# Kernel optimization log

Measured on AMD Instinct MI355X. Metric: run time of the kernel, lower is better.

Reference implementation:

```python
import jax, jax.numpy as jnp
import numpy as np

EPS = 1e-8  # CosineSimilarity eps
T = 0.5     # temperature


def _neg_indices(B):
    # static boolean mask removing diag and +/-B off-diagonals, as flat indices
    N = 2 * B
    m = np.eye(N) + np.eye(N, k=B) + np.eye(N, k=-B)
    mask = (1 - m).astype(bool)
    return np.nonzero(mask.ravel())[0]  # shape [N*(N-2)]


def setup_inputs() -> dict:
    key = jax.random.key(0)
    k1, k2 = jax.random.split(key)
    B, D = 4096, 128
    proj_i = jax.random.normal(k1, (B, D), dtype=jnp.float32)
    proj_j = jax.random.normal(k2, (B, D), dtype=jnp.float32)
    return {"proj_i": proj_i, "proj_j": proj_j}


def reference(proj_i, proj_j):
    B = proj_i.shape[0]
    N = 2 * B
    p = jnp.concatenate([proj_i, proj_j], axis=0)  # [N, D]
    # cosine sim of normalized vectors == dot product of unit vectors
    z = p / jnp.maximum(jnp.linalg.norm(p, axis=1, keepdims=True), EPS)
    sim = z @ z.T  # [N, N]
    pos = jnp.concatenate([jnp.diagonal(sim, offset=B), jnp.diagonal(sim, offset=-B)])  # [N]
    neg_idx = jnp.asarray(_neg_indices(B))
    neg = sim.ravel()[neg_idx].reshape(N, N - 2)
    logits = jnp.concatenate([pos[:, None], neg], axis=1) / T  # [N, N-1]
    # cross-entropy with label 0, sum reduction, divided by N
    logp = jax.nn.log_softmax(logits, axis=-1)
    loss = -jnp.sum(logp[:, 0]) / N
    return loss
```

## Files before the change

### kernel.cpp

```cpp
#include <hip/hip_runtime.h>
#include <hip/hip_bf16.h>

typedef __attribute__((ext_vector_type(8))) short short8;
typedef __attribute__((ext_vector_type(4))) float f32x4;

#define N_TOT 8192
#define HALF_B 4096
#define D 128
#define BM 128
#define BN 128
#define NQ 8
#define SLICE (N_TOT / NQ)
#define NSTEP (SLICE / BN)
#define SCALE 1.6986437f
#define CDIAG 7.3890561f

#if __has_builtin(__builtin_amdgcn_exp2f)
  #define EXP2(x) __builtin_amdgcn_exp2f(x)
#else
  #define EXP2(x) exp2f(x)
#endif

static __device__ inline unsigned short f2bf(float f) {
    unsigned int u = __builtin_bit_cast(unsigned int, f);
    u = (u + 0x7fffu + ((u >> 16) & 1u)) >> 16;
    return (unsigned short)u;
}

static __device__ __forceinline__ void gload16(const void* g, void* l) {
    __builtin_amdgcn_global_load_lds(
        (const __attribute__((address_space(1))) unsigned int*)g,
        (__attribute__((address_space(3))) unsigned int*)l, 16, 0, 0);
}

static __device__ __forceinline__ void stage_tile(const unsigned short* __restrict__ z,
                                                  int src_row, char* ldsbase, int tid) {
    int wv = tid >> 6, ln = tid & 63;
    const char* zb = (const char*)z;
    #pragma unroll
    for (int i = 0; i < 8; ++i) {
        int L  = wv * 8192 + i * 1024;
        int Ll = L + ln * 16;
        int r  = Ll >> 8;
        int c2 = (Ll & 255) ^ ((r & 15) << 4);
        gload16(zb + (size_t)(src_row + r) * 256 + c2, ldsbase + L);
    }
}

static __device__ __forceinline__ short8 ldsfrag(const char* ldsbase, int row, int kbyte) {
    int off = row * 256 + (kbyte ^ ((row & 15) << 4));
    return *reinterpret_cast<const short8*>(ldsbase + off);
}

__global__ __launch_bounds__(256) void nrm_k(const float* __restrict__ pi,
                                             const float* __restrict__ pj,
                                             unsigned short* __restrict__ z,
                                             float* __restrict__ ppos) {
    int tid = (int)threadIdx.x;
    int wid = tid >> 6, lane = tid & 63;
    int r = (int)blockIdx.x * 4 + wid;
    float2 va = *reinterpret_cast<const float2*>(pi + (size_t)r * D + lane * 2);
    float2 vb = *reinterpret_cast<const float2*>(pj + (size_t)r * D + lane * 2);
    float ssa = va.x * va.x + va.y * va.y;
    float ssb = vb.x * vb.x + vb.y * vb.y;
    float sab = va.x * vb.x + va.y * vb.y;
    #pragma unroll
    for (int off = 32; off >= 1; off >>= 1) {
        ssa += __shfl_xor(ssa, off);
        ssb += __shfl_xor(ssb, off);
        sab += __shfl_xor(sab, off);
    }
    float na = fmaxf(sqrtf(ssa), 1e-8f);
    float nb = fmaxf(sqrtf(ssb), 1e-8f);
    float inva = SCALE / na, invb = SCALE / nb;
    unsigned int pa = ((unsigned int)f2bf(va.y * inva) << 16) | (unsigned int)f2bf(va.x * inva);
    unsigned int pb = ((unsigned int)f2bf(vb.y * invb) << 16) | (unsigned int)f2bf(vb.x * invb);
    *reinterpret_cast<unsigned int*>(z + (size_t)r * D + lane * 2) = pa;
    *reinterpret_cast<unsigned int*>(z + (size_t)(r + HALF_B) * D + lane * 2) = pb;
    if (lane == 0) ppos[r] = 2.0f * sab / (na * nb);
}

__global__ __launch_bounds__(256, 2) void sim_k(const unsigned short* __restrict__ z,
                                                float* __restrict__ s_part) {
    __shared__ char lds[64 * 1024];
    char* Asm = lds;
    char* Bsm = lds + 32768;

    int tid  = (int)threadIdx.x;
    int lane = tid & 63;
    int wid  = tid >> 6;
    int lr   = lane & 15;
    int kg   = lane >> 4;
    int R0   = (int)blockIdx.x * BM;
    int C0   = (int)blockIdx.y * SLICE;

    stage_tile(z, R0, Asm, tid);
    stage_tile(z, C0, Bsm, tid);
    __syncthreads();

    short8 a[2][4];
    #pragma unroll
    for (int m = 0; m < 2; ++m)
        #pragma unroll
        for (int kt = 0; kt < 4; ++kt)
            a[m][kt] = ldsfrag(Asm, wid * 32 + m * 16 + lr, kg * 16 + kt * 64);

    float s[2][4];
    #pragma unroll
    for (int m = 0; m < 2; ++m)
        #pragma unroll
        for (int r = 0; r < 4; ++r) s[m][r] = 0.0f;

    for (int bs = 0; bs < NSTEP; ++bs) {
        if (bs) {
            __syncthreads();
            stage_tile(z, C0 + bs * BN, Bsm, tid);
            __syncthreads();
        }
        #pragma unroll
        for (int nt = 0; nt < 8; ++nt) {
            short8 b[4];
            #pragma unroll
            for (int kt = 0; kt < 4; ++kt)
                b[kt] = ldsfrag(Bsm, nt * 16 + lr, kg * 16 + kt * 64);
            #pragma unroll
            for (int m = 0; m < 2; ++m) {
                f32x4 acc = {0.0f, 0.0f, 0.0f, 0.0f};
                #pragma unroll
                for (int kt = 0; kt < 4; ++kt)
                    acc = __builtin_amdgcn_mfma_f32_16x16x32_bf16(a[m][kt], b[kt], acc, 0, 0, 0);
                #pragma unroll
                for (int r = 0; r < 4; ++r)
                    s[m][r] += EXP2(acc[r]);
            }
        }
    }

    #pragma unroll
    for (int off = 1; off <= 8; off <<= 1)
        #pragma unroll
        for (int m = 0; m < 2; ++m)
            #pragma unroll
            for (int r = 0; r < 4; ++r)
                s[m][r] += __shfl_xor(s[m][r], off);

    if (lr == 0) {
        int rowbase = R0 + wid * 32;
        #pragma unroll
        for (int m = 0; m < 2; ++m)
            #pragma unroll
            for (int r = 0; r < 4; ++r)
                s_part[(size_t)(rowbase + m * 16 + kg * 4 + r) * NQ + blockIdx.y] = s[m][r];
    }
}

__global__ __launch_bounds__(1024) void red_k(const float* __restrict__ s_part,
                                              const float* __restrict__ ppos,
                                              float* __restrict__ out) {
    int tid = (int)threadIdx.x;
    float acc = 0.0f;
    #pragma unroll
    for (int u = 0; u < 8; ++u) {
        int row = tid + u * 1024;
        f32x4 v0 = *reinterpret_cast<const f32x4*>(s_part + (size_t)row * NQ);
        f32x4 v1 = *reinterpret_cast<const f32x4*>(s_part + (size_t)row * NQ + 4);
        float S = (v0[0] + v0[1]) + (v0[2] + v0[3]) + (v1[0] + v1[1]) + (v1[2] + v1[3]);
        acc += __logf(S - CDIAG) - ppos[row & (HALF_B - 1)];
    }
    #pragma unroll
    for (int off = 32; off >= 1; off >>= 1) acc += __shfl_xor(acc, off);
    __shared__ float ls[16];
    if ((tid & 63) == 0) ls[tid >> 6] = acc;
    __syncthreads();
    if (tid < 16) {
        float w = ls[tid];
        #pragma unroll
        for (int off = 8; off >= 1; off >>= 1) w += __shfl_xor(w, off);
        if (tid == 0) out[0] = w * (1.0f / (float)N_TOT);
    }
}

extern "C" void kernel_launch(void* const* d_in, const int* in_sizes, int n_in,
                              void* d_out, int out_size, void* d_ws, size_t ws_size,
                              hipStream_t stream) {
    const float* pi = (const float*)d_in[0];
    const float* pj = (const float*)d_in[1];
    float* out = (float*)d_out;

    char* ws = (char*)d_ws;
    unsigned short* z = (unsigned short*)ws;
    float* ppos   = (float*)(ws + 2 * 1024 * 1024);
    float* s_part = (float*)(ws + 2 * 1024 * 1024 + 16 * 1024);

    nrm_k<<<dim3(1024), dim3(256), 0, stream>>>(pi, pj, z, ppos);
    sim_k<<<dim3(N_TOT / BM, NQ), dim3(256), 0, stream>>>(z, s_part);
    red_k<<<dim3(1), dim3(1024), 0, stream>>>(s_part, ppos, out);
}
```

Before: 32.23 us.

## Quantize normalized embeddings to FP8 e4m3 and use fp8 MFMA for similarity

The normalized, scaled embeddings are now stored as FP8 e4m3 instead of bf16, and the similarity GEMM uses the fp8 16x16x32 MFMA. This halves global and LDS traffic per tile and LDS footprint, which allows four blocks per CU, and the column split is doubled to 16 slices to raise grid parallelism. The cost is much lower precision in the dot products that feed exp2, which could push the loss past tolerance. The reduction kernel also reads twice as many partial sums per row.

```diff
diff --git a/kernel.cpp b/kernel.cpp
--- a/kernel.cpp
+++ b/kernel.cpp
@@ -1,7 +1,6 @@
 #include <hip/hip_runtime.h>
 #include <hip/hip_bf16.h>
 
-typedef __attribute__((ext_vector_type(8))) short short8;
 typedef __attribute__((ext_vector_type(4))) float f32x4;
 
 #define N_TOT 8192
@@ -9,7 +8,7 @@
 #define D 128
 #define BM 128
 #define BN 128
-#define NQ 8
+#define NQ 16
 #define SLICE (N_TOT / NQ)
 #define NSTEP (SLICE / BN)
 #define SCALE 1.6986437f
@@ -21,10 +20,22 @@
   #define EXP2(x) exp2f(x)
 #endif
 
-static __device__ inline unsigned short f2bf(float f) {
-    unsigned int u = __builtin_bit_cast(unsigned int, f);
-    u = (u + 0x7fffu + ((u >> 16) & 1u)) >> 16;
-    return (unsigned short)u;
+static __device__ __forceinline__ unsigned char f2e4m3(float x) {
+    unsigned int u = __builtin_bit_cast(unsigned int, x);
+    unsigned char s = (unsigned char)((u >> 24) & 0x80u);
+    unsigned int a = u & 0x7fffffffu;
+    float ax = __builtin_bit_cast(float, a);
+    if (ax >= 464.0f) return (unsigned char)(s | 0x7Eu);
+    int e = (int)(a >> 23) - 127;
+    if (e < -6) {
+        int n = (int)lrintf(ax * 512.0f);
+        return (unsigned char)(s | (unsigned char)n);
+    }
+    unsigned int m = a & 0x7fffffu;
+    unsigned int mr = m + 0x7FFFFu + ((m >> 20) & 1u);
+    if (mr >= 0x800000u) { mr = 0; ++e; }
+    if (e > 8) return (unsigned char)(s | 0x7Eu);
+    return (unsigned char)(s | (unsigned int)((e + 7) << 3) | (mr >> 20));
 }
 
 static __device__ __forceinline__ void gload16(const void* g, void* l) {
@@ -33,28 +44,27 @@
         (__attribute__((address_space(3))) unsigned int*)l, 16, 0, 0);
 }
 
-static __device__ __forceinline__ void stage_tile(const unsigned short* __restrict__ z,
-                                                  int src_row, char* ldsbase, int tid) {
+static __device__ __forceinline__ void stage_tile8(const unsigned char* __restrict__ z8,
+                                                   int src_row, char* ldsbase, int tid) {
     int wv = tid >> 6, ln = tid & 63;
-    const char* zb = (const char*)z;
-    #pragma unroll
-    for (int i = 0; i < 8; ++i) {
-        int L  = wv * 8192 + i * 1024;
+    #pragma unroll
+    for (int i = 0; i < 4; ++i) {
+        int L  = wv * 4096 + i * 1024;
         int Ll = L + ln * 16;
-        int r  = Ll >> 8;
-        int c2 = (Ll & 255) ^ ((r & 15) << 4);
-        gload16(zb + (size_t)(src_row + r) * 256 + c2, ldsbase + L);
-    }
-}
-
-static __device__ __forceinline__ short8 ldsfrag(const char* ldsbase, int row, int kbyte) {
-    int off = row * 256 + (kbyte ^ ((row & 15) << 4));
-    return *reinterpret_cast<const short8*>(ldsbase + off);
+        int r  = Ll >> 7;
+        int c2 = (Ll & 127) ^ ((r & 7) << 4);
+        gload16(z8 + (size_t)(src_row + r) * 128 + c2, ldsbase + L);
+    }
+}
+
+static __device__ __forceinline__ long ldsfrag8(const char* ldsbase, int row, int kbyte) {
+    int off = row * 128 + (kbyte ^ ((row & 7) << 4));
+    return *reinterpret_cast<const long*>(ldsbase + off);
 }
 
 __global__ __launch_bounds__(256) void nrm_k(const float* __restrict__ pi,
                                              const float* __restrict__ pj,
-                                             unsigned short* __restrict__ z,
+                                             unsigned char* __restrict__ z8,
                                              float* __restrict__ ppos) {
     int tid = (int)threadIdx.x;
     int wid = tid >> 6, lane = tid & 63;
@@ -73,18 +83,20 @@
     float na = fmaxf(sqrtf(ssa), 1e-8f);
     float nb = fmaxf(sqrtf(ssb), 1e-8f);
     float inva = SCALE / na, invb = SCALE / nb;
-    unsigned int pa = ((unsigned int)f2bf(va.y * inva) << 16) | (unsigned int)f2bf(va.x * inva);
-    unsigned int pb = ((unsigned int)f2bf(vb.y * invb) << 16) | (unsigned int)f2bf(vb.x * invb);
-    *reinterpret_cast<unsigned int*>(z + (size_t)r * D + lane * 2) = pa;
-    *reinterpret_cast<unsigned int*>(z + (size_t)(r + HALF_B) * D + lane * 2) = pb;
+    unsigned short qa = (unsigned short)f2e4m3(va.x * inva)
+                      | ((unsigned short)f2e4m3(va.y * inva) << 8);
+    unsigned short qb = (unsigned short)f2e4m3(vb.x * invb)
+                      | ((unsigned short)f2e4m3(vb.y * invb) << 8);
+    *reinterpret_cast<unsigned short*>(z8 + (size_t)r * D + lane * 2) = qa;
+    *reinterpret_cast<unsigned short*>(z8 + (size_t)(r + HALF_B) * D + lane * 2) = qb;
     if (lane == 0) ppos[r] = 2.0f * sab / (na * nb);
 }
 
-__global__ __launch_bounds__(256, 2) void sim_k(const unsigned short* __restrict__ z,
+__global__ __launch_bounds__(256, 4) void sim_k(const unsigned char* __restrict__ z8,
                                                 float* __restrict__ s_part) {
-    __shared__ char lds[64 * 1024];
+    __shared__ char lds[32 * 1024];
     char* Asm = lds;
-    char* Bsm = lds + 32768;
+    char* Bsm = lds + 16384;
 
     int tid  = (int)threadIdx.x;
     int lane = tid & 63;
@@ -94,16 +106,16 @@
     int R0   = (int)blockIdx.x * BM;
     int C0   = (int)blockIdx.y * SLICE;
 
-    stage_tile(z, R0, Asm, tid);
-    stage_tile(z, C0, Bsm, tid);
+    stage_tile8(z8, R0, Asm, tid);
+    stage_tile8(z8, C0, Bsm, tid);
     __syncthreads();
 
-    short8 a[2][4];
+    long a[2][4];
     #pragma unroll
     for (int m = 0; m < 2; ++m)
         #pragma unroll
         for (int kt = 0; kt < 4; ++kt)
-            a[m][kt] = ldsfrag(Asm, wid * 32 + m * 16 + lr, kg * 16 + kt * 64);
+            a[m][kt] = ldsfrag8(Asm, wid * 32 + m * 16 + lr, kg * 8 + kt * 32);
 
     float s[2][4];
     #pragma unroll
@@ -114,21 +126,21 @@
     for (int bs = 0; bs < NSTEP; ++bs) {
         if (bs) {
             __syncthreads();
-            stage_tile(z, C0 + bs * BN, Bsm, tid);
+            stage_tile8(z8, C0 + bs * BN, Bsm, tid);
             __syncthreads();
         }
         #pragma unroll
         for (int nt = 0; nt < 8; ++nt) {
-            short8 b[4];
+            long b[4];
             #pragma unroll
             for (int kt = 0; kt < 4; ++kt)
-                b[kt] = ldsfrag(Bsm, nt * 16 + lr, kg * 16 + kt * 64);
+                b[kt] = ldsfrag8(Bsm, nt * 16 + lr, kg * 8 + kt * 32);
             #pragma unroll
             for (int m = 0; m < 2; ++m) {
                 f32x4 acc = {0.0f, 0.0f, 0.0f, 0.0f};
                 #pragma unroll
                 for (int kt = 0; kt < 4; ++kt)
-                    acc = __builtin_amdgcn_mfma_f32_16x16x32_bf16(a[m][kt], b[kt], acc, 0, 0, 0);
+                    acc = __builtin_amdgcn_mfma_f32_16x16x32_fp8_fp8(a[m][kt], b[kt], acc, 0, 0, 0);
                 #pragma unroll
                 for (int r = 0; r < 4; ++r)
                     s[m][r] += EXP2(acc[r]);
@@ -162,9 +174,13 @@
     #pragma unroll
     for (int u = 0; u < 8; ++u) {
         int row = tid + u * 1024;
-        f32x4 v0 = *reinterpret_cast<const f32x4*>(s_part + (size_t)row * NQ);
-        f32x4 v1 = *reinterpret_cast<const f32x4*>(s_part + (size_t)row * NQ + 4);
-        float S = (v0[0] + v0[1]) + (v0[2] + v0[3]) + (v1[0] + v1[1]) + (v1[2] + v1[3]);
+        const f32x4* p = reinterpret_cast<const f32x4*>(s_part + (size_t)row * NQ);
+        float S = 0.0f;
+        #pragma unroll
+        for (int q = 0; q < 4; ++q) {
+            f32x4 v = p[q];
+            S += (v[0] + v[1]) + (v[2] + v[3]);
+        }
         acc += __logf(S - CDIAG) - ppos[row & (HALF_B - 1)];
     }
     #pragma unroll
@@ -188,11 +204,11 @@
     float* out = (float*)d_out;
 
     char* ws = (char*)d_ws;
-    unsigned short* z = (unsigned short*)ws;
-    float* ppos   = (float*)(ws + 2 * 1024 * 1024);
-    float* s_part = (float*)(ws + 2 * 1024 * 1024 + 16 * 1024);
-
-    nrm_k<<<dim3(1024), dim3(256), 0, stream>>>(pi, pj, z, ppos);
-    sim_k<<<dim3(N_TOT / BM, NQ), dim3(256), 0, stream>>>(z, s_part);
+    unsigned char* z8 = (unsigned char*)ws;
+    float* ppos   = (float*)(ws + 1024 * 1024);
+    float* s_part = (float*)(ws + 1024 * 1024 + 16 * 1024);
+
+    nrm_k<<<dim3(1024), dim3(256), 0, stream>>>(pi, pj, z8, ppos);
+    sim_k<<<dim3(N_TOT / BM, NQ), dim3(256), 0, stream>>>(z8, s_part);
     red_k<<<dim3(1), dim3(1024), 0, stream>>>(s_part, ppos, out);
 }
```

Result: slower. 34.64 us (+7.5%).

## Double-buffer B tiles in LDS and interleave MFMA chains

Applied to the files above, without the earlier changes.

Once the A fragments are in registers, the A LDS region is reused as a second B buffer, so the next column tile is prefetched with global_load_lds while the current one is consumed. Manual vmcnt waits and raw barriers replace the two __syncthreads per step. The two MFMA accumulator chains are interleaved and wrapped in s_setprio to hide MFMA dependency latency. The hand-written waitcnt values depend on the exact count of loads issued, which makes the code fragile if staging changes.

```diff
diff --git a/kernel.cpp b/kernel.cpp
--- a/kernel.cpp
+++ b/kernel.cpp
@@ -20,6 +20,9 @@
 #else
   #define EXP2(x) exp2f(x)
 #endif
+
+#define SBAR()   __builtin_amdgcn_s_barrier()
+#define SCHEDB() __builtin_amdgcn_sched_barrier(0)
 
 static __device__ inline unsigned short f2bf(float f) {
     unsigned int u = __builtin_bit_cast(unsigned int, f);
@@ -104,6 +107,9 @@
         #pragma unroll
         for (int kt = 0; kt < 4; ++kt)
             a[m][kt] = ldsfrag(Asm, wid * 32 + m * 16 + lr, kg * 16 + kt * 64);
+    __syncthreads();
+
+    stage_tile(z, C0 + BN, Asm, tid);
 
     float s[2][4];
     #pragma unroll
@@ -112,27 +118,38 @@
         for (int r = 0; r < 4; ++r) s[m][r] = 0.0f;
 
     for (int bs = 0; bs < NSTEP; ++bs) {
-        if (bs) {
-            __syncthreads();
-            stage_tile(z, C0 + bs * BN, Bsm, tid);
-            __syncthreads();
-        }
+        char* curb = (bs & 1) ? Asm : Bsm;
         #pragma unroll
         for (int nt = 0; nt < 8; ++nt) {
             short8 b[4];
             #pragma unroll
             for (int kt = 0; kt < 4; ++kt)
-                b[kt] = ldsfrag(Bsm, nt * 16 + lr, kg * 16 + kt * 64);
-            #pragma unroll
-            for (int m = 0; m < 2; ++m) {
-                f32x4 acc = {0.0f, 0.0f, 0.0f, 0.0f};
-                #pragma unroll
-                for (int kt = 0; kt < 4; ++kt)
-                    acc = __builtin_amdgcn_mfma_f32_16x16x32_bf16(a[m][kt], b[kt], acc, 0, 0, 0);
-                #pragma unroll
-                for (int r = 0; r < 4; ++r)
-                    s[m][r] += EXP2(acc[r]);
+                b[kt] = ldsfrag(curb, nt * 16 + lr, kg * 16 + kt * 64);
+            __builtin_amdgcn_s_setprio(1);
+            f32x4 acc0 = {0.0f, 0.0f, 0.0f, 0.0f};
+            f32x4 acc1 = {0.0f, 0.0f, 0.0f, 0.0f};
+            #pragma unroll
+            for (int kt = 0; kt < 4; ++kt) {
+                acc0 = __builtin_amdgcn_mfma_f32_16x16x32_bf16(a[0][kt], b[kt], acc0, 0, 0, 0);
+                acc1 = __builtin_amdgcn_mfma_f32_16x16x32_bf16(a[1][kt], b[kt], acc1, 0, 0, 0);
             }
+            __builtin_amdgcn_s_setprio(0);
+            #pragma unroll
+            for (int r = 0; r < 4; ++r) {
+                s[0][r] += EXP2(acc0[r]);
+                s[1][r] += EXP2(acc1[r]);
+            }
+        }
+        if (bs + 1 < NSTEP) {
+            SBAR(); SCHEDB();
+            if (bs + 2 < NSTEP) {
+                stage_tile(z, C0 + (bs + 2) * BN, curb, tid);
+                asm volatile("s_waitcnt vmcnt(8)" ::: "memory");
+            } else {
+                asm volatile("s_waitcnt vmcnt(0)" ::: "memory");
+            }
+            SCHEDB();
+            SBAR(); SCHEDB();
         }
     }
 
```

Result: no change. 32.65 us (+1.3%).
